# Optimization experiments

Hardware: AMD Instinct MI355X
Metric: run time of the kernel (lower is better)

## Reference

```python
import jax, jax.numpy as jnp
import numpy as np

B, S, D, H, E, K = 1, 4096, 1024, 4096, 8, 2


def setup_inputs() -> dict:
    key = jax.random.key(0)
    ks = jax.random.split(key, 10)
    scale = 0.02
    return {
        "hidden_states": jax.random.normal(ks[0], (B, S, D), dtype=jnp.float32),
        "gate_w": jax.random.normal(ks[1], (E, D), dtype=jnp.float32) * scale,
        "w_in": jax.random.normal(ks[2], (E, D, H), dtype=jnp.float32) * scale,
        "b_in": jnp.zeros((E, H), dtype=jnp.float32),
        "w_out": jax.random.normal(ks[3], (E, H, D), dtype=jnp.float32) * scale,
        "b_out": jnp.zeros((E, D), dtype=jnp.float32),
        "sw_in": jax.random.normal(ks[4], (D, H), dtype=jnp.float32) * scale,
        "sb_in": jnp.zeros((H,), dtype=jnp.float32),
        "sw_out": jax.random.normal(ks[5], (H, D), dtype=jnp.float32) * scale,
        "sb_out": jnp.zeros((D,), dtype=jnp.float32),
    }


def _ffn(x, w1, b1, w2, b2):
    # Linear -> exact (erf) GELU -> Linear, matching torch F.gelu default
    h = jax.nn.gelu(x @ w1 + b1, approximate=False)
    return h @ w2 + b2


def reference(hidden_states, gate_w, w_in, b_in, w_out, b_out,
              sw_in, sb_in, sw_out, sb_out):
    orig_shape = hidden_states.shape
    d = orig_shape[-1]
    x = hidden_states.reshape(-1, d)            # [T, D]
    T = x.shape[0]
    n_exp = gate_w.shape[0]

    # --- MoE gate: softmax over expert logits, top-k (sorted flag irrelevant
    # since the combine below is order-invariant) ---
    scores = jax.nn.softmax(x @ gate_w.T, axis=-1)        # [T, E]
    topk_w, topk_idx = jax.lax.top_k(scores, K)           # [T, K]

    # Per-token dense combine weights: w_tok[t, e] = sum of topk weights routed to e
    w_tok = jnp.zeros((T, n_exp), dtype=x.dtype).at[
        jnp.arange(T)[:, None], topk_idx].add(topk_w)     # [T, E]

    # --- expert dispatch + weighted combine (loop over small fixed E) ---
    y = jnp.zeros_like(x)
    for e in range(n_exp):
        y = y + w_tok[:, e:e + 1] * _ffn(x, w_in[e], b_in[e], w_out[e], b_out[e])

    # --- shared expert on the full (unflattened) input ---
    shared = _ffn(hidden_states, sw_in, sb_in, sw_out, sb_out)
    return y.reshape(orig_shape) + shared
```

## Files before the change

### kernel.cpp

```cpp
#include <hip/hip_runtime.h>
#include <hip/hip_bf16.h>
#include <math.h>


typedef unsigned short ushort_t;
typedef __attribute__((ext_vector_type(8))) __bf16 bf16x8;
typedef __attribute__((ext_vector_type(4))) float f32x4;

#define T_TOK 4096
#define DDIM  1024
#define HDIM  4096
#define NEXP  8
#define SLOT_PAD 10240
#define M_ALL (SLOT_PAD + T_TOK)

#define OFF_CNT   0u
#define OFF_OFFS  64u
#define OFF_TIDX  256u
#define OFF_TW    33024u
#define OFF_SLOT  65792u
#define OFF_TOK   98560u
#define OFF_XALL  1048576u
#define OFF_OUTS  OFF_XALL
#define OFF_WT    (OFF_XALL + 29360128u)
#define OFF_H     (OFF_WT + 75497472u)

__device__ __forceinline__ ushort_t f2b(float f) {
    __hip_bfloat16 h = __float2bfloat16(f);
    return *reinterpret_cast<ushort_t*>(&h);
}
__device__ __forceinline__ float b2f(ushort_t u) {
    __hip_bfloat16 h;
    *reinterpret_cast<ushort_t*>(&h) = u;
    return __bfloat162float(h);
}
__device__ __forceinline__ float gelu_fast(float v) {
    float u = 0.7978845608f * v * (1.0f + 0.044715f * v * v);
    float t = 1.0f - 2.0f / (__expf(2.0f * u) + 1.0f);
    return 0.5f * v * (1.0f + t);
}

__global__ void init_kernel(int* __restrict__ cnt, int* __restrict__ tok_of) {
    int i = blockIdx.x * 256 + threadIdx.x;
    if (i < 16) cnt[i] = 0;
    if (i < SLOT_PAD) tok_of[i] = -1;
}

__global__ void gate_kernel(const float* __restrict__ x, const float* __restrict__ gw,
                            int* __restrict__ tidx, float* __restrict__ tw,
                            int* __restrict__ cnt) {
    int t = blockIdx.x;
    int l = threadIdx.x;
    float acc[NEXP];
#pragma unroll
    for (int e = 0; e < NEXP; ++e) acc[e] = 0.f;
    for (int i = 0; i < DDIM / 64; ++i) {
        float xi = x[(size_t)t * DDIM + i * 64 + l];
#pragma unroll
        for (int e = 0; e < NEXP; ++e)
            acc[e] += xi * gw[e * DDIM + i * 64 + l];
    }
#pragma unroll
    for (int e = 0; e < NEXP; ++e)
        for (int off = 32; off; off >>= 1) acc[e] += __shfl_xor(acc[e], off);
    if (l == 0) {
        float m = acc[0];
#pragma unroll
        for (int e = 1; e < NEXP; ++e) m = fmaxf(m, acc[e]);
        float ex[NEXP], Z = 0.f;
#pragma unroll
        for (int e = 0; e < NEXP; ++e) { ex[e] = __expf(acc[e] - m); Z += ex[e]; }
        int b0 = 0;
#pragma unroll
        for (int e = 1; e < NEXP; ++e) if (ex[e] > ex[b0]) b0 = e;
        int b1 = (b0 == 0) ? 1 : 0;
#pragma unroll
        for (int e = 0; e < NEXP; ++e) if (e != b0 && ex[e] > ex[b1]) b1 = e;
        float inv = 1.0f / Z;
        tidx[2 * t] = b0; tidx[2 * t + 1] = b1;
        tw[2 * t] = ex[b0] * inv; tw[2 * t + 1] = ex[b1] * inv;
        atomicAdd(&cnt[b0], 1);
        atomicAdd(&cnt[b1], 1);
    }
}

__global__ void offs_kernel(const int* __restrict__ cnt, int* __restrict__ offs) {
    if (threadIdx.x == 0 && blockIdx.x == 0) {
        int o = 0;
#pragma unroll
        for (int e = 0; e < NEXP; ++e) {
            offs[e] = o;
            o += (cnt[e] + 255) & ~255;
        }
        offs[NEXP] = o;
    }
}

__global__ void assign_kernel(const int* __restrict__ tidx, const int* __restrict__ offs,
                              int* __restrict__ cur, int* __restrict__ slot_of,
                              int* __restrict__ tok_of) {
    int i = blockIdx.x * 256 + threadIdx.x;
    if (i >= 2 * T_TOK) return;
    int e = tidx[i];
    int s = offs[e] + atomicAdd(&cur[e], 1);
    slot_of[i] = s;
    tok_of[s] = i >> 1;
}

__global__ void build_x(const float* __restrict__ x, const int* __restrict__ tok_of,
                        const int* __restrict__ offs, ushort_t* __restrict__ Xall) {
    int b = blockIdx.x;
    int k = threadIdx.x * 4;
    int t;
    if (b < SLOT_PAD) {
        if (b >= offs[NEXP]) return;
        t = tok_of[b];
    } else {
        t = b - SLOT_PAD;
    }
    float4 v = make_float4(0.f, 0.f, 0.f, 0.f);
    if (t >= 0) v = *(const float4*)(x + (size_t)t * DDIM + k);
    ushort_t* p = Xall + (size_t)b * DDIM + k;
    p[0] = f2b(v.x); p[1] = f2b(v.y); p[2] = f2b(v.z); p[3] = f2b(v.w);
}

__global__ void transpose_cvt(const float* __restrict__ in, ushort_t* __restrict__ out,
                              int K, int N) {
    __shared__ float t[64][65];
    size_t zoff = (size_t)blockIdx.z * K * N;
    in += zoff; out += zoff;
    int k0 = blockIdx.x * 64, n0 = blockIdx.y * 64;
    int c = threadIdx.x & 63, r4 = threadIdx.x >> 6;
#pragma unroll
    for (int i = 0; i < 16; ++i) {
        int r = r4 + i * 4;
        t[r][c] = in[(size_t)(k0 + r) * N + n0 + c];
    }
    __syncthreads();
#pragma unroll
    for (int i = 0; i < 16; ++i) {
        int r = r4 + i * 4;
        out[(size_t)(n0 + r) * K + k0 + c] = f2b(t[c][r]);
    }
}

template <bool ACT_GELU, bool FFN2>
__global__ __launch_bounds__(1024, 4) void gemm_moe(
    const ushort_t* __restrict__ A, const ushort_t* __restrict__ WtBase,
    const float* __restrict__ bExp, const float* __restrict__ bSh,
    ushort_t* __restrict__ Cb, float* __restrict__ Cf,
    const int* __restrict__ offs, int N, int K) {
    int NMt = gridDim.x, NNt = gridDim.y;
    int flat = blockIdx.y * NMt + blockIdx.x;
    int xcd = flat & 7, rank = flat >> 3;
    int PM = NMt >> 2;
    int PN = NNt >> 1;
    int pm = xcd >> 1, pn = xcd & 1;
    int mi = pm * PM + rank / PN;
    int ni = pn * PN + rank % PN;
    int m0 = mi * 256, n0 = ni * 256;

    int e;
    if (m0 >= SLOT_PAD) {
        e = NEXP;
    } else {
        if (m0 >= offs[NEXP]) return;
        e = 0;
        while (offs[e + 1] <= m0) e++;
    }
    const ushort_t* Bt = WtBase + (size_t)e * N * K;
    const float* bias = (e == NEXP) ? bSh : bExp + (size_t)e * N;

    __shared__ ushort_t As[2][256 * 64];
    __shared__ ushort_t Bs[2][256 * 64];

    int tid = threadIdx.x;
    int lane = tid & 63, wid = tid >> 6;
    int wm = wid >> 2, wn = wid & 3;
    int q = lane >> 4, lr = lane & 15;

    size_t Aoff[2], Boff[2];
    int ldsOff[2];
#pragma unroll
    for (int it = 0; it < 2; ++it) {
        int L = it * 1024 + tid;
        int row = L >> 3;
        int c = (L & 7) ^ (row & 7);
        Aoff[it] = (size_t)(m0 + row) * K + c * 8;
        Boff[it] = (size_t)(n0 + row) * K + c * 8;
        ldsOff[it] = L * 8;
    }

    int rowA[4], rowB[4];
#pragma unroll
    for (int i = 0; i < 4; ++i) rowA[i] = wm * 64 + i * 16 + lr;
#pragma unroll
    for (int j = 0; j < 4; ++j) rowB[j] = wn * 64 + j * 16 + lr;

    f32x4 acc[4][4];
#pragma unroll
    for (int i = 0; i < 4; ++i)
#pragma unroll
        for (int j = 0; j < 4; ++j) acc[i][j] = (f32x4)(0.f);

    auto stage = [&](int kb, int buf) {
#pragma unroll
        for (int it = 0; it < 2; ++it) {
            __builtin_amdgcn_global_load_lds(
                (const __attribute__((address_space(1))) void*)(A + Aoff[it] + kb),
                (__attribute__((address_space(3))) void*)(&As[buf][ldsOff[it]]), 16, 0, 0);
            __builtin_amdgcn_global_load_lds(
                (const __attribute__((address_space(1))) void*)(Bt + Boff[it] + kb),
                (__attribute__((address_space(3))) void*)(&Bs[buf][ldsOff[it]]), 16, 0, 0);
        }
    };
    auto compute = [&](int buf) {
#pragma unroll
        for (int ks = 0; ks < 2; ++ks) {
            bf16x8 af[4], bfr[4];
#pragma unroll
            for (int i = 0; i < 4; ++i) {
                int cA = (ks * 4 + q) ^ (rowA[i] & 7);
                af[i] = *(const bf16x8*)(&As[buf][rowA[i] * 64 + cA * 8]);
            }
#pragma unroll
            for (int j = 0; j < 4; ++j) {
                int cB = (ks * 4 + q) ^ (rowB[j] & 7);
                bfr[j] = *(const bf16x8*)(&Bs[buf][rowB[j] * 64 + cB * 8]);
            }
#pragma unroll
            for (int i = 0; i < 4; ++i)
#pragma unroll
                for (int j = 0; j < 4; ++j)
                    acc[i][j] = __builtin_amdgcn_mfma_f32_16x16x32_bf16(
                        af[i], bfr[j], acc[i][j], 0, 0, 0);
        }
    };

    const int nk = K >> 6;
    stage(0, 0);
    int cur = 0;
    for (int t = 0; t < nk; ++t) {
        if (t + 1 < nk) {
            stage((t + 1) << 6, cur ^ 1);
            asm volatile("s_waitcnt vmcnt(4)" ::: "memory");
        } else {
            asm volatile("s_waitcnt vmcnt(0)" ::: "memory");
        }
        __builtin_amdgcn_s_barrier();
        compute(cur);
        __builtin_amdgcn_s_barrier();
        cur ^= 1;
    }

    int colb = n0 + wn * 64 + lr;
    int rowb = m0 + wm * 64 + q * 4;
#pragma unroll
    for (int j = 0; j < 4; ++j) {
        int col = colb + j * 16;
        float bz = bias[col];
#pragma unroll
        for (int i = 0; i < 4; ++i) {
            int row = rowb + i * 16;
#pragma unroll
            for (int r = 0; r < 4; ++r) {
                float v = acc[i][j][r] + bz;
                if (ACT_GELU) v = gelu_fast(v);
                if (!FFN2 || e < NEXP)
                    Cb[(size_t)(row + r) * N + col] = f2b(v);
                else
                    Cf[(size_t)(row + r - SLOT_PAD) * N + col] = v;
            }
        }
    }
}

__global__ void combine_kernel(float* __restrict__ out, const ushort_t* __restrict__ OutS,
                               const int* __restrict__ slot_of, const float* __restrict__ tw) {
    int t = blockIdx.x;
    int d = threadIdx.x * 4;
    int s0 = slot_of[2 * t], s1 = slot_of[2 * t + 1];
    float w0 = tw[2 * t], w1 = tw[2 * t + 1];
    float* po = out + (size_t)t * DDIM + d;
    float4 o = *(float4*)po;
    const ushort_t* p0 = OutS + (size_t)s0 * DDIM + d;
    const ushort_t* p1 = OutS + (size_t)s1 * DDIM + d;
    o.x += w0 * b2f(p0[0]) + w1 * b2f(p1[0]);
    o.y += w0 * b2f(p0[1]) + w1 * b2f(p1[1]);
    o.z += w0 * b2f(p0[2]) + w1 * b2f(p1[2]);
    o.w += w0 * b2f(p0[3]) + w1 * b2f(p1[3]);
    *(float4*)po = o;
}

extern "C" void kernel_launch(void* const* d_in, const int* in_sizes, int n_in,
                              void* d_out, int out_size, void* d_ws, size_t ws_size,
                              hipStream_t stream) {
    const float* x      = (const float*)d_in[0];
    const float* gw     = (const float*)d_in[1];
    const float* w_in   = (const float*)d_in[2];
    const float* b_in   = (const float*)d_in[3];
    const float* w_out  = (const float*)d_in[4];
    const float* b_out  = (const float*)d_in[5];
    const float* sw_in  = (const float*)d_in[6];
    const float* sb_in  = (const float*)d_in[7];
    const float* sw_out = (const float*)d_in[8];
    const float* sb_out = (const float*)d_in[9];
    float* out = (float*)d_out;

    char* ws = (char*)d_ws;
    int*      cnt     = (int*)(ws + OFF_CNT);
    int*      offs    = (int*)(ws + OFF_OFFS);
    int*      tidx    = (int*)(ws + OFF_TIDX);
    float*    tw      = (float*)(ws + OFF_TW);
    int*      slot_of = (int*)(ws + OFF_SLOT);
    int*      tok_of  = (int*)(ws + OFF_TOK);
    ushort_t* Xall    = (ushort_t*)(ws + OFF_XALL);
    ushort_t* OutS    = (ushort_t*)(ws + OFF_OUTS);
    ushort_t* Wt      = (ushort_t*)(ws + OFF_WT);
    ushort_t* Hbuf    = (ushort_t*)(ws + OFF_H);

    init_kernel<<<(SLOT_PAD + 255) / 256, 256, 0, stream>>>(cnt, tok_of);
    gate_kernel<<<T_TOK, 64, 0, stream>>>(x, gw, tidx, tw, cnt);
    offs_kernel<<<1, 64, 0, stream>>>(cnt, offs);
    assign_kernel<<<(2 * T_TOK + 255) / 256, 256, 0, stream>>>(tidx, offs, cnt + 8,
                                                               slot_of, tok_of);
    build_x<<<M_ALL, 256, 0, stream>>>(x, tok_of, offs, Xall);

    transpose_cvt<<<dim3(DDIM / 64, HDIM / 64, NEXP), 256, 0, stream>>>(w_in, Wt, DDIM, HDIM);
    transpose_cvt<<<dim3(DDIM / 64, HDIM / 64, 1), 256, 0, stream>>>(
        sw_in, Wt + (size_t)NEXP * HDIM * DDIM, DDIM, HDIM);
    gemm_moe<true, false><<<dim3(M_ALL / 256, HDIM / 256), 1024, 0, stream>>>(
        Xall, Wt, b_in, sb_in, Hbuf, nullptr, offs, HDIM, DDIM);

    transpose_cvt<<<dim3(HDIM / 64, DDIM / 64, NEXP), 256, 0, stream>>>(w_out, Wt, HDIM, DDIM);
    transpose_cvt<<<dim3(HDIM / 64, DDIM / 64, 1), 256, 0, stream>>>(
        sw_out, Wt + (size_t)NEXP * HDIM * DDIM, HDIM, DDIM);
    gemm_moe<false, true><<<dim3(M_ALL / 256, DDIM / 256), 1024, 0, stream>>>(
        Hbuf, Wt, b_out, sb_out, OutS, out, offs, DDIM, HDIM);

    combine_kernel<<<T_TOK, 256, 0, stream>>>(out, OutS, slot_of, tw);
    (void)in_sizes; (void)n_in; (void)out_size; (void)ws_size;
}
```

Measured before the change: 573.5 us.

## Retile MoE GEMM to 256x128 tiles with K=32 triple-buffered pipeline

The grouped GEMM moves from 1024-thread 256x256 tiles with K=64 double buffering to 512-thread 256x128 tiles with K=32 slices in a three-stage LDS ring. Each wave now computes a 128x32 sub-tile, issuing its A fragment loads in two halves, and raises wave priority around the MFMA bursts. The aim is to cut LDS use and register pressure so more blocks fit per CU, and to hide load latency behind a deeper prefetch. In exchange each loaded A tile feeds fewer output columns, K iterations double along with their barriers, and the wrapped prefetch index issues redundant loads on the last two iterations.

```diff
diff --git a/kernel.cpp b/kernel.cpp
--- a/kernel.cpp
+++ b/kernel.cpp
@@ -145,7 +145,7 @@
 }
 
 template <bool ACT_GELU, bool FFN2>
-__global__ __launch_bounds__(1024, 4) void gemm_moe(
+__global__ __launch_bounds__(512, 4) void gemm_moe(
     const ushort_t* __restrict__ A, const ushort_t* __restrict__ WtBase,
     const float* __restrict__ bExp, const float* __restrict__ bSh,
     ushort_t* __restrict__ Cb, float* __restrict__ Cf,
@@ -158,7 +158,7 @@
     int pm = xcd >> 1, pn = xcd & 1;
     int mi = pm * PM + rank / PN;
     int ni = pn * PN + rank % PN;
-    int m0 = mi * 256, n0 = ni * 256;
+    int m0 = mi * 256, n0 = ni * 128;
 
     int e;
     if (m0 >= SLOT_PAD) {
@@ -171,96 +171,112 @@
     const ushort_t* Bt = WtBase + (size_t)e * N * K;
     const float* bias = (e == NEXP) ? bSh : bExp + (size_t)e * N;
 
-    __shared__ ushort_t As[2][256 * 64];
-    __shared__ ushort_t Bs[2][256 * 64];
+    __shared__ ushort_t As[3][256 * 32];
+    __shared__ ushort_t Bs[3][128 * 32];
 
     int tid = threadIdx.x;
     int lane = tid & 63, wid = tid >> 6;
     int wm = wid >> 2, wn = wid & 3;
     int q = lane >> 4, lr = lane & 15;
 
-    size_t Aoff[2], Boff[2];
-    int ldsOff[2];
+    size_t AoffG[2], BoffG;
+    int AoffL[2], BoffL;
 #pragma unroll
     for (int it = 0; it < 2; ++it) {
-        int L = it * 1024 + tid;
-        int row = L >> 3;
-        int c = (L & 7) ^ (row & 7);
-        Aoff[it] = (size_t)(m0 + row) * K + c * 8;
-        Boff[it] = (size_t)(n0 + row) * K + c * 8;
-        ldsOff[it] = L * 8;
-    }
-
-    int rowA[4], rowB[4];
-#pragma unroll
-    for (int i = 0; i < 4; ++i) rowA[i] = wm * 64 + i * 16 + lr;
-#pragma unroll
-    for (int j = 0; j < 4; ++j) rowB[j] = wn * 64 + j * 16 + lr;
-
-    f32x4 acc[4][4];
-#pragma unroll
-    for (int i = 0; i < 4; ++i)
-#pragma unroll
-        for (int j = 0; j < 4; ++j) acc[i][j] = (f32x4)(0.f);
-
-    auto stage = [&](int kb, int buf) {
-#pragma unroll
-        for (int it = 0; it < 2; ++it) {
-            __builtin_amdgcn_global_load_lds(
-                (const __attribute__((address_space(1))) void*)(A + Aoff[it] + kb),
-                (__attribute__((address_space(3))) void*)(&As[buf][ldsOff[it]]), 16, 0, 0);
-            __builtin_amdgcn_global_load_lds(
-                (const __attribute__((address_space(1))) void*)(Bt + Boff[it] + kb),
-                (__attribute__((address_space(3))) void*)(&Bs[buf][ldsOff[it]]), 16, 0, 0);
-        }
+        int L = it * 512 + tid;
+        int r = L >> 2;
+        int u = (L & 3) ^ ((r >> 1) & 3);
+        AoffG[it] = (size_t)(m0 + r) * K + u * 8;
+        AoffL[it] = L * 8;
+    }
+    {
+        int L = tid;
+        int r = L >> 2;
+        int u = (L & 3) ^ ((r >> 1) & 3);
+        BoffG = (size_t)(n0 + r) * K + u * 8;
+        BoffL = L * 8;
+    }
+
+    f32x4 acc[8][2];
+#pragma unroll
+    for (int i = 0; i < 8; ++i)
+#pragma unroll
+        for (int j = 0; j < 2; ++j) acc[i][j] = (f32x4)(0.f);
+
+    auto stage = [&](int kb, int b) {
+        __builtin_amdgcn_global_load_lds(
+            (const __attribute__((address_space(1))) void*)(A + AoffG[0] + kb),
+            (__attribute__((address_space(3))) void*)(&As[b][AoffL[0]]), 16, 0, 0);
+        __builtin_amdgcn_global_load_lds(
+            (const __attribute__((address_space(1))) void*)(A + AoffG[1] + kb),
+            (__attribute__((address_space(3))) void*)(&As[b][AoffL[1]]), 16, 0, 0);
+        __builtin_amdgcn_global_load_lds(
+            (const __attribute__((address_space(1))) void*)(Bt + BoffG + kb),
+            (__attribute__((address_space(3))) void*)(&Bs[b][BoffL]), 16, 0, 0);
     };
-    auto compute = [&](int buf) {
-#pragma unroll
-        for (int ks = 0; ks < 2; ++ks) {
-            bf16x8 af[4], bfr[4];
-#pragma unroll
-            for (int i = 0; i < 4; ++i) {
-                int cA = (ks * 4 + q) ^ (rowA[i] & 7);
-                af[i] = *(const bf16x8*)(&As[buf][rowA[i] * 64 + cA * 8]);
-            }
-#pragma unroll
-            for (int j = 0; j < 4; ++j) {
-                int cB = (ks * 4 + q) ^ (rowB[j] & 7);
-                bfr[j] = *(const bf16x8*)(&Bs[buf][rowB[j] * 64 + cB * 8]);
-            }
-#pragma unroll
-            for (int i = 0; i < 4; ++i)
-#pragma unroll
-                for (int j = 0; j < 4; ++j)
-                    acc[i][j] = __builtin_amdgcn_mfma_f32_16x16x32_bf16(
-                        af[i], bfr[j], acc[i][j], 0, 0, 0);
-        }
+    auto compute = [&](int b) {
+        const ushort_t* Ab = &As[b][0];
+        const ushort_t* Bb = &Bs[b][0];
+        bf16x8 bfr[2];
+#pragma unroll
+        for (int j = 0; j < 2; ++j) {
+            int r = wn * 32 + j * 16 + lr;
+            int c = q ^ ((r >> 1) & 3);
+            bfr[j] = *(const bf16x8*)(Bb + r * 32 + c * 8);
+        }
+        bf16x8 af[4];
+#pragma unroll
+        for (int i = 0; i < 4; ++i) {
+            int r = wm * 128 + i * 16 + lr;
+            int c = q ^ ((r >> 1) & 3);
+            af[i] = *(const bf16x8*)(Ab + r * 32 + c * 8);
+        }
+        __builtin_amdgcn_s_setprio(1);
+#pragma unroll
+        for (int i = 0; i < 4; ++i)
+#pragma unroll
+            for (int j = 0; j < 2; ++j)
+                acc[i][j] = __builtin_amdgcn_mfma_f32_16x16x32_bf16(
+                    af[i], bfr[j], acc[i][j], 0, 0, 0);
+#pragma unroll
+        for (int i = 0; i < 4; ++i) {
+            int r = wm * 128 + (i + 4) * 16 + lr;
+            int c = q ^ ((r >> 1) & 3);
+            af[i] = *(const bf16x8*)(Ab + r * 32 + c * 8);
+        }
+#pragma unroll
+        for (int i = 0; i < 4; ++i)
+#pragma unroll
+            for (int j = 0; j < 2; ++j)
+                acc[i + 4][j] = __builtin_amdgcn_mfma_f32_16x16x32_bf16(
+                    af[i], bfr[j], acc[i + 4][j], 0, 0, 0);
+        __builtin_amdgcn_s_setprio(0);
     };
 
-    const int nk = K >> 6;
+    const int nk = K >> 5;
     stage(0, 0);
-    int cur = 0;
+    stage(1 << 5, 1);
+    int bc = 0, bs = 2;
     for (int t = 0; t < nk; ++t) {
-        if (t + 1 < nk) {
-            stage((t + 1) << 6, cur ^ 1);
-            asm volatile("s_waitcnt vmcnt(4)" ::: "memory");
-        } else {
-            asm volatile("s_waitcnt vmcnt(0)" ::: "memory");
-        }
+        int kn = t + 2;
+        if (kn >= nk) kn -= nk;
+        stage(kn << 5, bs);
+        asm volatile("s_waitcnt vmcnt(6)" ::: "memory");
         __builtin_amdgcn_s_barrier();
-        compute(cur);
+        compute(bc);
         __builtin_amdgcn_s_barrier();
-        cur ^= 1;
-    }
-
-    int colb = n0 + wn * 64 + lr;
-    int rowb = m0 + wm * 64 + q * 4;
-#pragma unroll
-    for (int j = 0; j < 4; ++j) {
+        bc = (bc == 2) ? 0 : bc + 1;
+        bs = (bs == 2) ? 0 : bs + 1;
+    }
+
+    int colb = n0 + wn * 32 + lr;
+    int rowb = m0 + wm * 128 + q * 4;
+#pragma unroll
+    for (int j = 0; j < 2; ++j) {
         int col = colb + j * 16;
         float bz = bias[col];
 #pragma unroll
-        for (int i = 0; i < 4; ++i) {
+        for (int i = 0; i < 8; ++i) {
             int row = rowb + i * 16;
 #pragma unroll
             for (int r = 0; r < 4; ++r) {
@@ -329,13 +345,13 @@
     transpose_cvt<<<dim3(DDIM / 64, HDIM / 64, NEXP), 256, 0, stream>>>(w_in, Wt, DDIM, HDIM);
     transpose_cvt<<<dim3(DDIM / 64, HDIM / 64, 1), 256, 0, stream>>>(
         sw_in, Wt + (size_t)NEXP * HDIM * DDIM, DDIM, HDIM);
-    gemm_moe<true, false><<<dim3(M_ALL / 256, HDIM / 256), 1024, 0, stream>>>(
+    gemm_moe<true, false><<<dim3(M_ALL / 256, HDIM / 128), 512, 0, stream>>>(
         Xall, Wt, b_in, sb_in, Hbuf, nullptr, offs, HDIM, DDIM);
 
     transpose_cvt<<<dim3(HDIM / 64, DDIM / 64, NEXP), 256, 0, stream>>>(w_out, Wt, HDIM, DDIM);
     transpose_cvt<<<dim3(HDIM / 64, DDIM / 64, 1), 256, 0, stream>>>(
         sw_out, Wt + (size_t)NEXP * HDIM * DDIM, HDIM, DDIM);
-    gemm_moe<false, true><<<dim3(M_ALL / 256, DDIM / 256), 1024, 0, stream>>>(
+    gemm_moe<false, true><<<dim3(M_ALL / 256, DDIM / 128), 512, 0, stream>>>(
         Hbuf, Wt, b_out, sb_out, OutS, out, offs, DDIM, HDIM);
 
     combine_kernel<<<T_TOK, 256, 0, stream>>>(out, OutS, slot_of, tw);
```

Result: slower. 588.8 us (+2.7%).

## Restructure MoE GEMM into 8-wave ping-pong pipeline with half-tile staging

Applied to the files above, without the earlier changes.

Reworks the 256x256 GEMM from 16 waves with simple double buffering into 8 waves, each owning a 128x64 sub-tile. The main loop is split into phases that interleave half-tile global-to-LDS loads with MFMA groups, using barriers, s_setprio and sched_barrier to overlap memory and compute. B fragments are reused across four phases to cut LDS reads. The aim is to hide load latency and raise MFMA utilisation, at the cost of much higher register pressure (32 accumulators per thread) and a more fragile wait-count schedule.

```diff
diff --git a/kernel.cpp b/kernel.cpp
--- a/kernel.cpp
+++ b/kernel.cpp
@@ -144,8 +144,42 @@
     }
 }
 
+#define PHASE(SLOT, Q, STAGE, WAIT)                                          \
+    {                                                                        \
+        const ushort_t* Ah = &As[SLOT][wm][0];                               \
+        const ushort_t* Bh = &Bs[SLOT][wn >> 1][0];                          \
+        if ((Q) == 0) {                                                      \
+            _Pragma("unroll") for (int nf = 0; nf < 4; ++nf)                 \
+            _Pragma("unroll") for (int ks = 0; ks < 2; ++ks) {               \
+                int r = (wn & 1) * 64 + nf * 16 + lr;                        \
+                int c = ((ks << 2) + q4) ^ (r & 7);                          \
+                bfr[nf][ks] = *(const bf16x8*)(Bh + r * 64 + c * 8);         \
+            }                                                                \
+        }                                                                    \
+        bf16x8 af[2][2];                                                     \
+        _Pragma("unroll") for (int d = 0; d < 2; ++d)                        \
+        _Pragma("unroll") for (int ks = 0; ks < 2; ++ks) {                   \
+            int r = (2 * (Q) + d) * 16 + lr;                                 \
+            int c = ((ks << 2) + q4) ^ (r & 7);                              \
+            af[d][ks] = *(const bf16x8*)(Ah + r * 64 + c * 8);               \
+        }                                                                    \
+        STAGE;                                                               \
+        if (WAIT) asm volatile("s_waitcnt vmcnt(4)" ::: "memory");           \
+        __builtin_amdgcn_s_barrier();                                        \
+        asm volatile("s_waitcnt lgkmcnt(0)" ::: "memory");                   \
+        __builtin_amdgcn_sched_barrier(0);                                   \
+        __builtin_amdgcn_s_setprio(1);                                       \
+        _Pragma("unroll") for (int d = 0; d < 2; ++d)                        \
+        _Pragma("unroll") for (int nf = 0; nf < 4; ++nf)                     \
+        _Pragma("unroll") for (int ks = 0; ks < 2; ++ks)                     \
+            acc[2 * (Q) + d][nf] = __builtin_amdgcn_mfma_f32_16x16x32_bf16(  \
+                af[d][ks], bfr[nf][ks], acc[2 * (Q) + d][nf], 0, 0, 0);      \
+        __builtin_amdgcn_s_setprio(0);                                       \
+        __builtin_amdgcn_s_barrier();                                        \
+    }
+
 template <bool ACT_GELU, bool FFN2>
-__global__ __launch_bounds__(1024, 4) void gemm_moe(
+__global__ __launch_bounds__(512, 2) void gemm_moe(
     const ushort_t* __restrict__ A, const ushort_t* __restrict__ WtBase,
     const float* __restrict__ bExp, const float* __restrict__ bSh,
     ushort_t* __restrict__ Cb, float* __restrict__ Cf,
@@ -171,100 +205,90 @@
     const ushort_t* Bt = WtBase + (size_t)e * N * K;
     const float* bias = (e == NEXP) ? bSh : bExp + (size_t)e * N;
 
-    __shared__ ushort_t As[2][256 * 64];
-    __shared__ ushort_t Bs[2][256 * 64];
+    __shared__ ushort_t As[2][2][128 * 64];
+    __shared__ ushort_t Bs[2][2][128 * 64];
 
     int tid = threadIdx.x;
     int lane = tid & 63, wid = tid >> 6;
     int wm = wid >> 2, wn = wid & 3;
-    int q = lane >> 4, lr = lane & 15;
-
-    size_t Aoff[2], Boff[2];
-    int ldsOff[2];
-#pragma unroll
-    for (int it = 0; it < 2; ++it) {
-        int L = it * 1024 + tid;
-        int row = L >> 3;
-        int c = (L & 7) ^ (row & 7);
-        Aoff[it] = (size_t)(m0 + row) * K + c * 8;
-        Boff[it] = (size_t)(n0 + row) * K + c * 8;
-        ldsOff[it] = L * 8;
-    }
-
-    int rowA[4], rowB[4];
-#pragma unroll
-    for (int i = 0; i < 4; ++i) rowA[i] = wm * 64 + i * 16 + lr;
-#pragma unroll
-    for (int j = 0; j < 4; ++j) rowB[j] = wn * 64 + j * 16 + lr;
-
-    f32x4 acc[4][4];
-#pragma unroll
-    for (int i = 0; i < 4; ++i)
+    int q4 = lane >> 4, lr = lane & 15;
+
+    int srow = tid >> 3;
+    int sc = ((tid & 7) ^ (srow & 7)) * 8;
+    size_t aB[2][2], bB[2][2];
+    int ldsI[2];
+#pragma unroll
+    for (int h = 0; h < 2; ++h)
+#pragma unroll
+        for (int it = 0; it < 2; ++it) {
+            aB[h][it] = (size_t)(m0 + h * 128 + it * 64 + srow) * K + sc;
+            bB[h][it] = (size_t)(n0 + h * 128 + it * 64 + srow) * K + sc;
+        }
+#pragma unroll
+    for (int it = 0; it < 2; ++it) ldsI[it] = (it * 512 + tid) * 8;
+
+    auto stA = [&](int kb, int slot, int h) {
+#pragma unroll
+        for (int it = 0; it < 2; ++it)
+            __builtin_amdgcn_global_load_lds(
+                (const __attribute__((address_space(1))) void*)(A + aB[h][it] + kb),
+                (__attribute__((address_space(3))) void*)(&As[slot][h][ldsI[it]]),
+                16, 0, 0);
+    };
+    auto stB = [&](int kb, int slot, int h) {
+#pragma unroll
+        for (int it = 0; it < 2; ++it)
+            __builtin_amdgcn_global_load_lds(
+                (const __attribute__((address_space(1))) void*)(Bt + bB[h][it] + kb),
+                (__attribute__((address_space(3))) void*)(&Bs[slot][h][ldsI[it]]),
+                16, 0, 0);
+    };
+
+    f32x4 acc[8][4];
+#pragma unroll
+    for (int i = 0; i < 8; ++i)
 #pragma unroll
         for (int j = 0; j < 4; ++j) acc[i][j] = (f32x4)(0.f);
 
-    auto stage = [&](int kb, int buf) {
-#pragma unroll
-        for (int it = 0; it < 2; ++it) {
-            __builtin_amdgcn_global_load_lds(
-                (const __attribute__((address_space(1))) void*)(A + Aoff[it] + kb),
-                (__attribute__((address_space(3))) void*)(&As[buf][ldsOff[it]]), 16, 0, 0);
-            __builtin_amdgcn_global_load_lds(
-                (const __attribute__((address_space(1))) void*)(Bt + Boff[it] + kb),
-                (__attribute__((address_space(3))) void*)(&Bs[buf][ldsOff[it]]), 16, 0, 0);
-        }
-    };
-    auto compute = [&](int buf) {
-#pragma unroll
-        for (int ks = 0; ks < 2; ++ks) {
-            bf16x8 af[4], bfr[4];
-#pragma unroll
-            for (int i = 0; i < 4; ++i) {
-                int cA = (ks * 4 + q) ^ (rowA[i] & 7);
-                af[i] = *(const bf16x8*)(&As[buf][rowA[i] * 64 + cA * 8]);
-            }
-#pragma unroll
-            for (int j = 0; j < 4; ++j) {
-                int cB = (ks * 4 + q) ^ (rowB[j] & 7);
-                bfr[j] = *(const bf16x8*)(&Bs[buf][rowB[j] * 64 + cB * 8]);
-            }
-#pragma unroll
-            for (int i = 0; i < 4; ++i)
-#pragma unroll
-                for (int j = 0; j < 4; ++j)
-                    acc[i][j] = __builtin_amdgcn_mfma_f32_16x16x32_bf16(
-                        af[i], bfr[j], acc[i][j], 0, 0, 0);
-        }
-    };
-
     const int nk = K >> 6;
-    stage(0, 0);
-    int cur = 0;
-    for (int t = 0; t < nk; ++t) {
-        if (t + 1 < nk) {
-            stage((t + 1) << 6, cur ^ 1);
-            asm volatile("s_waitcnt vmcnt(4)" ::: "memory");
-        } else {
-            asm volatile("s_waitcnt vmcnt(0)" ::: "memory");
-        }
-        __builtin_amdgcn_s_barrier();
-        compute(cur);
-        __builtin_amdgcn_s_barrier();
-        cur ^= 1;
-    }
+    const int nk2 = nk >> 1;
+
+    stB(0, 0, 0); stB(0, 0, 1);
+    stA(0, 0, 0); stA(0, 0, 1);
+    stB(64, 1, 0); stB(64, 1, 1);
+    asm volatile("s_waitcnt vmcnt(4)" ::: "memory");
+    __builtin_amdgcn_s_barrier();
+
+    for (int i = 0; i < nk2; ++i) {
+        int t1 = 2 * i + 1;
+        int t2 = 2 * i + 2; if (t2 >= nk) t2 -= nk;
+        int t3 = 2 * i + 3; if (t3 >= nk) t3 -= nk;
+        int k1 = t1 << 6, k2 = t2 << 6, k3 = t3 << 6;
+        bf16x8 bfr[4][2];
+
+        PHASE(0, 0, stA(k1, 1, 0), false)
+        PHASE(0, 1, stA(k1, 1, 1), false)
+        PHASE(0, 2, stB(k2, 0, 0), false)
+        PHASE(0, 3, stB(k2, 0, 1), true)
+        PHASE(1, 0, stA(k2, 0, 0), false)
+        PHASE(1, 1, stA(k2, 0, 1), false)
+        PHASE(1, 2, stB(k3, 1, 0), false)
+        PHASE(1, 3, stB(k3, 1, 1), true)
+    }
+    asm volatile("s_waitcnt vmcnt(0)" ::: "memory");
 
     int colb = n0 + wn * 64 + lr;
-    int rowb = m0 + wm * 64 + q * 4;
-#pragma unroll
-    for (int j = 0; j < 4; ++j) {
-        int col = colb + j * 16;
+    int rowb = m0 + wm * 128 + q4 * 4;
+#pragma unroll
+    for (int nf = 0; nf < 4; ++nf) {
+        int col = colb + nf * 16;
         float bz = bias[col];
 #pragma unroll
-        for (int i = 0; i < 4; ++i) {
-            int row = rowb + i * 16;
+        for (int mf = 0; mf < 8; ++mf) {
+            int row = rowb + mf * 16;
 #pragma unroll
             for (int r = 0; r < 4; ++r) {
-                float v = acc[i][j][r] + bz;
+                float v = acc[mf][nf][r] + bz;
                 if (ACT_GELU) v = gelu_fast(v);
                 if (!FFN2 || e < NEXP)
                     Cb[(size_t)(row + r) * N + col] = f2b(v);
@@ -329,13 +353,13 @@
     transpose_cvt<<<dim3(DDIM / 64, HDIM / 64, NEXP), 256, 0, stream>>>(w_in, Wt, DDIM, HDIM);
     transpose_cvt<<<dim3(DDIM / 64, HDIM / 64, 1), 256, 0, stream>>>(
         sw_in, Wt + (size_t)NEXP * HDIM * DDIM, DDIM, HDIM);
-    gemm_moe<true, false><<<dim3(M_ALL / 256, HDIM / 256), 1024, 0, stream>>>(
+    gemm_moe<true, false><<<dim3(M_ALL / 256, HDIM / 256), 512, 0, stream>>>(
         Xall, Wt, b_in, sb_in, Hbuf, nullptr, offs, HDIM, DDIM);
 
     transpose_cvt<<<dim3(HDIM / 64, DDIM / 64, NEXP), 256, 0, stream>>>(w_out, Wt, HDIM, DDIM);
     transpose_cvt<<<dim3(HDIM / 64, DDIM / 64, 1), 256, 0, stream>>>(
         sw_out, Wt + (size_t)NEXP * HDIM * DDIM, HDIM, DDIM);
-    gemm_moe<false, true><<<dim3(M_ALL / 256, DDIM / 256), 1024, 0, stream>>>(
+    gemm_moe<false, true><<<dim3(M_ALL / 256, DDIM / 256), 512, 0, stream>>>(
         Hbuf, Wt, b_out, sb_out, OutS, out, offs, DDIM, HDIM);
 
     combine_kernel<<<T_TOK, 256, 0, stream>>>(out, OutS, slot_of, tw);
```

New measurement: 642.2 us. +12.0%, slower.

## Merge routing and transpose launches and vectorize GEMM epilogue via swapped MFMA operands

Applied to the files above, without the earlier changes.

Removes the init and offs kernels by zeroing counters with a memset and computing expert offsets inside assign_kernel. build_x now masks pad slots by comparing against per-expert counts, so tok_of no longer needs to be reset to -1. The expert and shared weight transposes are merged into one launch per layer. The MFMA operands are swapped so each lane holds four consecutive columns, which lets the epilogue use vector bias loads and packed 8-byte bf16 or 16-byte fp32 stores instead of scalar strided stores.

```diff
diff --git a/kernel.cpp b/kernel.cpp
--- a/kernel.cpp
+++ b/kernel.cpp
@@ -40,12 +40,6 @@
     return 0.5f * v * (1.0f + t);
 }
 
-__global__ void init_kernel(int* __restrict__ cnt, int* __restrict__ tok_of) {
-    int i = blockIdx.x * 256 + threadIdx.x;
-    if (i < 16) cnt[i] = 0;
-    if (i < SLOT_PAD) tok_of[i] = -1;
-}
-
 __global__ void gate_kernel(const float* __restrict__ x, const float* __restrict__ gw,
                             int* __restrict__ tidx, float* __restrict__ tw,
                             int* __restrict__ cnt) {
@@ -84,37 +78,36 @@
     }
 }
 
-__global__ void offs_kernel(const int* __restrict__ cnt, int* __restrict__ offs) {
-    if (threadIdx.x == 0 && blockIdx.x == 0) {
-        int o = 0;
-#pragma unroll
-        for (int e = 0; e < NEXP; ++e) {
-            offs[e] = o;
-            o += (cnt[e] + 255) & ~255;
-        }
-        offs[NEXP] = o;
-    }
-}
-
-__global__ void assign_kernel(const int* __restrict__ tidx, const int* __restrict__ offs,
-                              int* __restrict__ cur, int* __restrict__ slot_of,
-                              int* __restrict__ tok_of) {
+__global__ void assign_kernel(const int* __restrict__ tidx, const int* __restrict__ cnt,
+                              int* __restrict__ cur, int* __restrict__ offs,
+                              int* __restrict__ slot_of, int* __restrict__ tok_of) {
+    int off[NEXP + 1];
+    off[0] = 0;
+#pragma unroll
+    for (int e = 0; e < NEXP; ++e) off[e + 1] = off[e] + ((cnt[e] + 255) & ~255);
     int i = blockIdx.x * 256 + threadIdx.x;
+    if (i == 0) {
+#pragma unroll
+        for (int e = 0; e <= NEXP; ++e) offs[e] = off[e];
+    }
     if (i >= 2 * T_TOK) return;
     int e = tidx[i];
-    int s = offs[e] + atomicAdd(&cur[e], 1);
+    int s = off[e] + atomicAdd(&cur[e], 1);
     slot_of[i] = s;
     tok_of[s] = i >> 1;
 }
 
 __global__ void build_x(const float* __restrict__ x, const int* __restrict__ tok_of,
-                        const int* __restrict__ offs, ushort_t* __restrict__ Xall) {
+                        const int* __restrict__ offs, const int* __restrict__ cnt,
+                        ushort_t* __restrict__ Xall) {
     int b = blockIdx.x;
     int k = threadIdx.x * 4;
     int t;
     if (b < SLOT_PAD) {
         if (b >= offs[NEXP]) return;
-        t = tok_of[b];
+        int e = 0;
+        while (offs[e + 1] <= b) e++;
+        t = (b - offs[e] < cnt[e]) ? tok_of[b] : -1;
     } else {
         t = b - SLOT_PAD;
     }
@@ -124,11 +117,12 @@
     p[0] = f2b(v.x); p[1] = f2b(v.y); p[2] = f2b(v.z); p[3] = f2b(v.w);
 }
 
-__global__ void transpose_cvt(const float* __restrict__ in, ushort_t* __restrict__ out,
-                              int K, int N) {
+__global__ void transpose_cvt9(const float* __restrict__ w, const float* __restrict__ sw,
+                               ushort_t* __restrict__ out, int K, int N) {
     __shared__ float t[64][65];
-    size_t zoff = (size_t)blockIdx.z * K * N;
-    in += zoff; out += zoff;
+    int z = blockIdx.z;
+    const float* in = (z < NEXP) ? w + (size_t)z * K * N : sw;
+    out += (size_t)z * K * N;
     int k0 = blockIdx.x * 64, n0 = blockIdx.y * 64;
     int c = threadIdx.x & 63, r4 = threadIdx.x >> 6;
 #pragma unroll
@@ -233,7 +227,7 @@
 #pragma unroll
                 for (int j = 0; j < 4; ++j)
                     acc[i][j] = __builtin_amdgcn_mfma_f32_16x16x32_bf16(
-                        af[i], bfr[j], acc[i][j], 0, 0, 0);
+                        bfr[j], af[i], acc[i][j], 0, 0, 0);
         }
     };
 
@@ -253,23 +247,34 @@
         cur ^= 1;
     }
 
-    int colb = n0 + wn * 64 + lr;
-    int rowb = m0 + wm * 64 + q * 4;
-#pragma unroll
-    for (int j = 0; j < 4; ++j) {
-        int col = colb + j * 16;
-        float bz = bias[col];
-#pragma unroll
-        for (int i = 0; i < 4; ++i) {
-            int row = rowb + i * 16;
-#pragma unroll
-            for (int r = 0; r < 4; ++r) {
-                float v = acc[i][j][r] + bz;
-                if (ACT_GELU) v = gelu_fast(v);
-                if (!FFN2 || e < NEXP)
-                    Cb[(size_t)(row + r) * N + col] = f2b(v);
-                else
-                    Cf[(size_t)(row + r - SLOT_PAD) * N + col] = v;
+    int colb = n0 + wn * 64 + q * 4;
+    int rowb = m0 + wm * 64 + lr;
+    float4 bz[4];
+#pragma unroll
+    for (int nj = 0; nj < 4; ++nj)
+        bz[nj] = *(const float4*)(bias + colb + nj * 16);
+#pragma unroll
+    for (int mi = 0; mi < 4; ++mi) {
+        int row = rowb + mi * 16;
+#pragma unroll
+        for (int nj = 0; nj < 4; ++nj) {
+            float v0 = acc[mi][nj][0] + bz[nj].x;
+            float v1 = acc[mi][nj][1] + bz[nj].y;
+            float v2 = acc[mi][nj][2] + bz[nj].z;
+            float v3 = acc[mi][nj][3] + bz[nj].w;
+            if (ACT_GELU) {
+                v0 = gelu_fast(v0); v1 = gelu_fast(v1);
+                v2 = gelu_fast(v2); v3 = gelu_fast(v3);
+            }
+            int col = colb + nj * 16;
+            if (!FFN2 || e < NEXP) {
+                uint2 u;
+                u.x = (unsigned)f2b(v0) | ((unsigned)f2b(v1) << 16);
+                u.y = (unsigned)f2b(v2) | ((unsigned)f2b(v3) << 16);
+                *(uint2*)(Cb + (size_t)row * N + col) = u;
+            } else {
+                float4 f = make_float4(v0, v1, v2, v3);
+                *(float4*)(Cf + (size_t)(row - SLOT_PAD) * N + col) = f;
             }
         }
     }
@@ -319,22 +324,19 @@
     ushort_t* Wt      = (ushort_t*)(ws + OFF_WT);
     ushort_t* Hbuf    = (ushort_t*)(ws + OFF_H);
 
-    init_kernel<<<(SLOT_PAD + 255) / 256, 256, 0, stream>>>(cnt, tok_of);
+    hipMemsetAsync(cnt, 0, 64, stream);
     gate_kernel<<<T_TOK, 64, 0, stream>>>(x, gw, tidx, tw, cnt);
-    offs_kernel<<<1, 64, 0, stream>>>(cnt, offs);
-    assign_kernel<<<(2 * T_TOK + 255) / 256, 256, 0, stream>>>(tidx, offs, cnt + 8,
-                                                               slot_of, tok_of);
-    build_x<<<M_ALL, 256, 0, stream>>>(x, tok_of, offs, Xall);
-
-    transpose_cvt<<<dim3(DDIM / 64, HDIM / 64, NEXP), 256, 0, stream>>>(w_in, Wt, DDIM, HDIM);
-    transpose_cvt<<<dim3(DDIM / 64, HDIM / 64, 1), 256, 0, stream>>>(
-        sw_in, Wt + (size_t)NEXP * HDIM * DDIM, DDIM, HDIM);
+    assign_kernel<<<(2 * T_TOK + 255) / 256, 256, 0, stream>>>(tidx, cnt, cnt + 8,
+                                                               offs, slot_of, tok_of);
+    build_x<<<M_ALL, 256, 0, stream>>>(x, tok_of, offs, cnt, Xall);
+
+    transpose_cvt9<<<dim3(DDIM / 64, HDIM / 64, NEXP + 1), 256, 0, stream>>>(
+        w_in, sw_in, Wt, DDIM, HDIM);
     gemm_moe<true, false><<<dim3(M_ALL / 256, HDIM / 256), 1024, 0, stream>>>(
         Xall, Wt, b_in, sb_in, Hbuf, nullptr, offs, HDIM, DDIM);
 
-    transpose_cvt<<<dim3(HDIM / 64, DDIM / 64, NEXP), 256, 0, stream>>>(w_out, Wt, HDIM, DDIM);
-    transpose_cvt<<<dim3(HDIM / 64, DDIM / 64, 1), 256, 0, stream>>>(
-        sw_out, Wt + (size_t)NEXP * HDIM * DDIM, HDIM, DDIM);
+    transpose_cvt9<<<dim3(HDIM / 64, DDIM / 64, NEXP + 1), 256, 0, stream>>>(
+        w_out, sw_out, Wt, HDIM, DDIM);
     gemm_moe<false, true><<<dim3(M_ALL / 256, DDIM / 256), 1024, 0, stream>>>(
         Hbuf, Wt, b_out, sb_out, OutS, out, offs, DDIM, HDIM);
 
```

Result: faster. 554.4 us (-3.3%).
